# Performance work log

Hardware: AMD Instinct MI355X
Metric: run time of the kernel (lower is better)

## Reference

```python
import jax, jax.numpy as jnp
import numpy as np
import math

FIRE_THRESH = 0.85
SQRT_2_OVER_PI = math.sqrt(2.0 / math.pi)

def _gelu(x):
    # tanh-approx GELU, exactly as in the torch module
    return 0.5 * x * (1.0 + jnp.tanh(SQRT_2_OVER_PI * (x + 0.044715 * x * x * x)))

def setup_inputs() -> dict:
    key = jax.random.key(0)
    ks = jax.random.split(key, 8)
    B, T, D, N = 8, 4096, 1024, 512
    x = jax.random.normal(ks[0], (B, T, D), dtype=jnp.float32)
    log_beta = jnp.asarray(math.log(10.0), dtype=jnp.float32)
    log_k_inject = jnp.asarray(math.log(0.1), dtype=jnp.float32)
    # buffer keys are stored L2-normalized in the original module
    raw_keys = jax.random.normal(ks[1], (N, D), dtype=jnp.float32)
    buf_keys = raw_keys / jnp.maximum(jnp.linalg.norm(raw_keys, axis=-1, keepdims=True), 1e-12)
    buf_vals = jax.random.normal(ks[2], (N, D), dtype=jnp.float32)
    global_sum = jax.random.normal(ks[3], (D,), dtype=jnp.float32)
    mask = jnp.ones((N,), dtype=bool)
    hit_count = jax.random.randint(ks[4], (N,), 0, 100, dtype=jnp.int64 if jax.config.jax_enable_x64 else jnp.int32)
    n_global = 300
    return {"x": x, "log_beta": log_beta, "log_k_inject": log_k_inject,
            "buf_keys": buf_keys, "buf_vals": buf_vals, "global_sum": global_sum,
            "mask": mask, "hit_count": hit_count, "n_global": n_global}

def reference(x, log_beta, log_k_inject, buf_keys, buf_vals, global_sum, mask, hit_count, n_global):
    B, T, D = x.shape
    y = _gelu(x)  # [B,T,D]
    # m_curr = mean over all tokens, detached in the original
    m_curr = jax.lax.stop_gradient(jnp.mean(y.reshape(-1, D), axis=0))  # [D]
    beta = jnp.clip(jnp.exp(log_beta), 1.0, 50.0)
    k_inject = jnp.clip(jnp.exp(log_k_inject), 0.001, 2.0)
    # retrieval (no_grad block in torch)
    q = m_curr / jnp.maximum(jnp.linalg.norm(m_curr), 1e-12)  # [D]
    sims = buf_keys @ q                                        # [N]
    logits = jnp.where(mask, beta * sims, -1e9)
    attn = jax.nn.softmax(logits, axis=0)
    retrieved = attn @ buf_vals                                # [D]
    nearest_idx = jnp.argmax(logits)
    sims_plain = jnp.where(mask, sims, -1.0)
    hit = hit_count[nearest_idx] + (sims_plain[nearest_idx] > FIRE_THRESH).astype(hit_count.dtype)
    t = k_inject * jnp.log(hit.astype(x.dtype) + 1.0)
    global_mean = global_sum / max(int(n_global), 1)
    delta = jax.lax.stop_gradient(retrieved - global_mean)     # [D]
    return y + t * delta.reshape(1, 1, D)
```

## Files before the change

kernel.cpp:

```cpp
#include <hip/hip_runtime.h>
#include <math.h>

#define ROWS 32768
#define D    1024
#define DF4  256
#define NKEYS 512
#define CSB  512
#define CSR  64
#define R1B  16
#define RETB 8

__device__ __forceinline__ float gelu1(float x) {
    float z = 0.7978845608028654f * fmaf(0.044715f * x, x * x, x);
    float e = __expf(2.0f * z);
    return x - x / (e + 1.0f);
}

__global__ __launch_bounds__(256) void k_colsum(const float4* __restrict__ x4,
                                                float4* __restrict__ partial4) {
    int t = threadIdx.x, b = blockIdx.x;
    const float4* p = x4 + (size_t)b * CSR * DF4 + t;
    float4 acc = make_float4(0.f, 0.f, 0.f, 0.f);
#pragma unroll 8
    for (int r = 0; r < CSR; ++r) {
        float4 v = p[(size_t)r * DF4];
        acc.x += gelu1(v.x); acc.y += gelu1(v.y);
        acc.z += gelu1(v.z); acc.w += gelu1(v.w);
    }
    partial4[(size_t)b * DF4 + t] = acc;
}

__global__ __launch_bounds__(1024) void k_red1(const float* __restrict__ partial,
                                               float* __restrict__ partial2) {
    int d = threadIdx.x, b = blockIdx.x;
    float s = 0.f;
#pragma unroll
    for (int p = 0; p < 32; ++p) s += partial[(size_t)(b * 32 + p) * D + d];
    partial2[b * D + d] = s;
}

__global__ __launch_bounds__(1024) void k_q(const float* __restrict__ partial2,
                                            float* __restrict__ q) {
    __shared__ float red[1024];
    int d = threadIdx.x;
    float s = 0.f;
#pragma unroll
    for (int p = 0; p < R1B; ++p) s += partial2[p * D + d];
    float m = s * (1.0f / 32768.0f);
    red[d] = m * m;
    __syncthreads();
    for (int st = 512; st > 0; st >>= 1) {
        if (d < st) red[d] += red[d + st];
        __syncthreads();
    }
    float inv = 1.0f / fmaxf(sqrtf(red[0]), 1e-12f);
    q[d] = m * inv;
}

__global__ __launch_bounds__(256) void k_sims(const float4* __restrict__ keys4,
                                              const float4* __restrict__ q4,
                                              float* __restrict__ sims) {
    int n = blockIdx.x, t = threadIdx.x;
    float4 k = keys4[(size_t)n * DF4 + t];
    float4 qq = q4[t];
    float v = k.x * qq.x + k.y * qq.y + k.z * qq.z + k.w * qq.w;
#pragma unroll
    for (int off = 32; off > 0; off >>= 1) v += __shfl_down(v, off, 64);
    __shared__ float wsum[4];
    int wave = t >> 6, lane = t & 63;
    if (lane == 0) wsum[wave] = v;
    __syncthreads();
    if (t == 0) sims[n] = wsum[0] + wsum[1] + wsum[2] + wsum[3];
}

__global__ __launch_bounds__(256) void k_ret(const float* __restrict__ sims,
                                             const float4* __restrict__ vals4,
                                             const float* __restrict__ log_beta,
                                             const float* __restrict__ log_kinj,
                                             const int* __restrict__ hit_count,
                                             float* __restrict__ tval,
                                             float4* __restrict__ rp4) {
    int t = threadIdx.x, b = blockIdx.x;
    float beta = fminf(fmaxf(__expf(log_beta[0]), 1.0f), 50.0f);
    float s0 = sims[t], s1 = sims[t + 256];
    float l0 = beta * s0, l1 = beta * s1;

    __shared__ float red[256];
    red[t] = fmaxf(l0, l1);
    __syncthreads();
    for (int st = 128; st > 0; st >>= 1) {
        if (t < st) red[t] = fmaxf(red[t], red[t + st]);
        __syncthreads();
    }
    float lmax = red[0];
    __syncthreads();
    float e0 = __expf(l0 - lmax), e1 = __expf(l1 - lmax);
    red[t] = e0 + e1;
    __syncthreads();
    for (int st = 128; st > 0; st >>= 1) {
        if (t < st) red[t] += red[t + st];
        __syncthreads();
    }
    float inv_sum = 1.0f / red[0];
    __shared__ float w[NKEYS];
    w[t] = e0 * inv_sum;
    w[t + 256] = e1 * inv_sum;
    __syncthreads();

    if (b == 0) {
        __shared__ float amv[256];
        __shared__ int   ami[256];
        float v; int i;
        if (l1 > l0) { v = l1; i = t + 256; } else { v = l0; i = t; }
        amv[t] = v; ami[t] = i;
        __syncthreads();
        for (int st = 128; st > 0; st >>= 1) {
            if (t < st) {
                float ov = amv[t + st]; int oi = ami[t + st];
                if (ov > amv[t] || (ov == amv[t] && oi < ami[t])) { amv[t] = ov; ami[t] = oi; }
            }
            __syncthreads();
        }
        if (t == 0) {
            int nearest = ami[0];
            float sp = sims[nearest];
            int hit = hit_count[nearest] + (sp > 0.85f ? 1 : 0);
            float kinj = fminf(fmaxf(__expf(log_kinj[0]), 0.001f), 2.0f);
            tval[0] = kinj * logf((float)hit + 1.0f);
        }
    }

    float4 acc = make_float4(0.f, 0.f, 0.f, 0.f);
#pragma unroll 8
    for (int j = 0; j < 64; ++j) {
        int n = b * 64 + j;
        float a = w[n];
        float4 v = vals4[(size_t)n * DF4 + t];
        acc.x = fmaf(a, v.x, acc.x); acc.y = fmaf(a, v.y, acc.y);
        acc.z = fmaf(a, v.z, acc.z); acc.w = fmaf(a, v.w, acc.w);
    }
    rp4[(size_t)b * DF4 + t] = acc;
}

__global__ __launch_bounds__(256) void k_out(const float4* __restrict__ x4,
                                             const float4* __restrict__ rp4,
                                             const float4* __restrict__ gsum4,
                                             const int* __restrict__ ngl,
                                             const float* __restrict__ tval,
                                             float4* __restrict__ out4) {
    const int NF4 = ROWS * DF4;
    int i0 = blockIdx.x * 256 + threadIdx.x;
    int stride = gridDim.x * 256;
    int c = i0 & (DF4 - 1);

    float rx = 0.f, ry = 0.f, rz = 0.f, rw = 0.f;
#pragma unroll
    for (int bb = 0; bb < RETB; ++bb) {
        float4 v = rp4[bb * DF4 + c];
        rx += v.x; ry += v.y; rz += v.z; rw += v.w;
    }
    int ng = ngl[0];
    float invn = 1.0f / (float)(ng > 1 ? ng : 1);
    float tv = tval[0];
    float4 g = gsum4[c];
    float ax = tv * (rx - g.x * invn);
    float ay = tv * (ry - g.y * invn);
    float az = tv * (rz - g.z * invn);
    float aw = tv * (rw - g.w * invn);

    for (int i = i0; i < NF4; i += stride) {
        float4 v = x4[i];
        float4 o;
        o.x = gelu1(v.x) + ax;
        o.y = gelu1(v.y) + ay;
        o.z = gelu1(v.z) + az;
        o.w = gelu1(v.w) + aw;
        out4[i] = o;
    }
}

extern "C" void kernel_launch(void* const* d_in, const int* in_sizes, int n_in,
                              void* d_out, int out_size, void* d_ws, size_t ws_size,
                              hipStream_t stream) {
    const float* x          = (const float*)d_in[0];
    const float* log_beta   = (const float*)d_in[1];
    const float* log_kinj   = (const float*)d_in[2];
    const float* buf_keys   = (const float*)d_in[3];
    const float* buf_vals   = (const float*)d_in[4];
    const float* global_sum = (const float*)d_in[5];
    const int*   hit_count  = (const int*)d_in[7];
    const int*   n_global   = (const int*)d_in[8];
    float* out = (float*)d_out;

    float* ws = (float*)d_ws;
    float* partial  = ws;
    float* partial2 = partial + (size_t)CSB * D;
    float* q        = partial2 + R1B * D;
    float* sims     = q + D;
    float* tval     = sims + NKEYS;
    float* rp       = tval + 4;

    k_colsum<<<CSB, 256, 0, stream>>>((const float4*)x, (float4*)partial);
    k_red1 <<<R1B, 1024, 0, stream>>>(partial, partial2);
    k_q    <<<1, 1024, 0, stream>>>(partial2, q);
    k_sims <<<NKEYS, 256, 0, stream>>>((const float4*)buf_keys, (const float4*)q, sims);
    k_ret  <<<RETB, 256, 0, stream>>>(sims, (const float4*)buf_vals,
                                      log_beta, log_kinj, hit_count, tval, (float4*)rp);
    k_out  <<<2048, 256, 0, stream>>>((const float4*)x, (const float4*)rp,
                                      (const float4*)global_sum, n_global, tval,
                                      (float4*)out);
}
```

Before: 90.77 us.

## Cache GELU output as fp16 in first pass and fuse q normalization into sims

The first pass now writes GELU(x) as fp16 to workspace while computing column sums, and the output kernel reads these half values instead of re-reading fp32 x and recomputing GELU. This trades reading 128MB of x for writing and then reading 64MB of fp16, and drops the second GELU evaluation. It also merges the q normalization kernel into the similarity kernel, which removes one launch but recomputes the norm in every block. The fp16 storage of y adds rounding error to the output, and the new path runs only when the workspace is large enough.

```diff
diff --git a/kernel.cpp b/kernel.cpp
--- a/kernel.cpp
+++ b/kernel.cpp
@@ -1,4 +1,5 @@
 #include <hip/hip_runtime.h>
+#include <hip/hip_fp16.h>
 #include <math.h>
 
 #define ROWS 32768
@@ -14,6 +15,32 @@
     float z = 0.7978845608028654f * fmaf(0.044715f * x, x * x, x);
     float e = __expf(2.0f * z);
     return x - x / (e + 1.0f);
+}
+
+__device__ __forceinline__ short4 pack4(float a, float b, float c, float d) {
+    short4 r;
+    r.x = (short)__half_as_ushort(__float2half_rn(a));
+    r.y = (short)__half_as_ushort(__float2half_rn(b));
+    r.z = (short)__half_as_ushort(__float2half_rn(c));
+    r.w = (short)__half_as_ushort(__float2half_rn(d));
+    return r;
+}
+
+__global__ __launch_bounds__(256) void k_colsum_y(const float4* __restrict__ x4,
+                                                  float4* __restrict__ partial4,
+                                                  short4* __restrict__ y4) {
+    int t = threadIdx.x, b = blockIdx.x;
+    const float4* p = x4 + (size_t)b * CSR * DF4 + t;
+    short4* yp = y4 + (size_t)b * CSR * DF4 + t;
+    float4 acc = make_float4(0.f, 0.f, 0.f, 0.f);
+#pragma unroll 4
+    for (int r = 0; r < CSR; ++r) {
+        float4 v = p[(size_t)r * DF4];
+        float g0 = gelu1(v.x), g1 = gelu1(v.y), g2 = gelu1(v.z), g3 = gelu1(v.w);
+        acc.x += g0; acc.y += g1; acc.z += g2; acc.w += g3;
+        yp[(size_t)r * DF4] = pack4(g0, g1, g2, g3);
+    }
+    partial4[(size_t)b * DF4 + t] = acc;
 }
 
 __global__ __launch_bounds__(256) void k_colsum(const float4* __restrict__ x4,
@@ -39,38 +66,35 @@
     partial2[b * D + d] = s;
 }
 
-__global__ __launch_bounds__(1024) void k_q(const float* __restrict__ partial2,
-                                            float* __restrict__ q) {
-    __shared__ float red[1024];
-    int d = threadIdx.x;
-    float s = 0.f;
-#pragma unroll
-    for (int p = 0; p < R1B; ++p) s += partial2[p * D + d];
-    float m = s * (1.0f / 32768.0f);
-    red[d] = m * m;
-    __syncthreads();
-    for (int st = 512; st > 0; st >>= 1) {
-        if (d < st) red[d] += red[d + st];
-        __syncthreads();
-    }
-    float inv = 1.0f / fmaxf(sqrtf(red[0]), 1e-12f);
-    q[d] = m * inv;
-}
-
-__global__ __launch_bounds__(256) void k_sims(const float4* __restrict__ keys4,
-                                              const float4* __restrict__ q4,
+__global__ __launch_bounds__(256) void k_simq(const float4* __restrict__ partial2_4,
+                                              const float4* __restrict__ keys4,
                                               float* __restrict__ sims) {
     int n = blockIdx.x, t = threadIdx.x;
+    int wave = t >> 6, lane = t & 63;
+    float4 m4 = make_float4(0.f, 0.f, 0.f, 0.f);
+#pragma unroll
+    for (int p = 0; p < R1B; ++p) {
+        float4 v = partial2_4[p * DF4 + t];
+        m4.x += v.x; m4.y += v.y; m4.z += v.z; m4.w += v.w;
+    }
+    const float sc = 1.0f / 32768.0f;
+    m4.x *= sc; m4.y *= sc; m4.z *= sc; m4.w *= sc;
     float4 k = keys4[(size_t)n * DF4 + t];
-    float4 qq = q4[t];
-    float v = k.x * qq.x + k.y * qq.y + k.z * qq.z + k.w * qq.w;
-#pragma unroll
-    for (int off = 32; off > 0; off >>= 1) v += __shfl_down(v, off, 64);
-    __shared__ float wsum[4];
-    int wave = t >> 6, lane = t & 63;
-    if (lane == 0) wsum[wave] = v;
-    __syncthreads();
-    if (t == 0) sims[n] = wsum[0] + wsum[1] + wsum[2] + wsum[3];
+    float n2 = m4.x*m4.x + m4.y*m4.y + m4.z*m4.z + m4.w*m4.w;
+    float kd = k.x*m4.x + k.y*m4.y + k.z*m4.z + k.w*m4.w;
+#pragma unroll
+    for (int off = 32; off > 0; off >>= 1) {
+        n2 += __shfl_down(n2, off, 64);
+        kd += __shfl_down(kd, off, 64);
+    }
+    __shared__ float wn[4], wk[4];
+    if (lane == 0) { wn[wave] = n2; wk[wave] = kd; }
+    __syncthreads();
+    if (t == 0) {
+        float tn = wn[0] + wn[1] + wn[2] + wn[3];
+        float tk = wk[0] + wk[1] + wk[2] + wk[3];
+        sims[n] = tk / fmaxf(sqrtf(tn), 1e-12f);
+    }
 }
 
 __global__ __launch_bounds__(256) void k_ret(const float* __restrict__ sims,
@@ -133,26 +157,73 @@
     float4 acc = make_float4(0.f, 0.f, 0.f, 0.f);
 #pragma unroll 8
     for (int j = 0; j < 64; ++j) {
-        int n = b * 64 + j;
-        float a = w[n];
-        float4 v = vals4[(size_t)n * DF4 + t];
+        int nn = b * 64 + j;
+        float a = w[nn];
+        float4 v = vals4[(size_t)nn * DF4 + t];
         acc.x = fmaf(a, v.x, acc.x); acc.y = fmaf(a, v.y, acc.y);
         acc.z = fmaf(a, v.z, acc.z); acc.w = fmaf(a, v.w, acc.w);
     }
     rp4[(size_t)b * DF4 + t] = acc;
 }
 
-__global__ __launch_bounds__(256) void k_out(const float4* __restrict__ x4,
-                                             const float4* __restrict__ rp4,
-                                             const float4* __restrict__ gsum4,
-                                             const int* __restrict__ ngl,
-                                             const float* __restrict__ tval,
-                                             float4* __restrict__ out4) {
+__global__ __launch_bounds__(256) void k_out_y(const int4* __restrict__ y8,
+                                               const float4* __restrict__ rp4,
+                                               const float4* __restrict__ gsum4,
+                                               const int* __restrict__ ngl,
+                                               const float* __restrict__ tval,
+                                               float4* __restrict__ out4) {
+    const int NG = ROWS * 128;
+    int g0 = blockIdx.x * 256 + threadIdx.x;
+    int stride = gridDim.x * 256;
+    int c0 = (2 * g0) & (DF4 - 1);
+    int c1 = c0 + 1;
+
+    float4 r0 = make_float4(0.f,0.f,0.f,0.f), r1 = make_float4(0.f,0.f,0.f,0.f);
+#pragma unroll
+    for (int bb = 0; bb < RETB; ++bb) {
+        float4 a = rp4[bb * DF4 + c0];
+        float4 c = rp4[bb * DF4 + c1];
+        r0.x += a.x; r0.y += a.y; r0.z += a.z; r0.w += a.w;
+        r1.x += c.x; r1.y += c.y; r1.z += c.z; r1.w += c.w;
+    }
+    int ng = ngl[0];
+    float invn = 1.0f / (float)(ng > 1 ? ng : 1);
+    float tv = tval[0];
+    float4 gA = gsum4[c0], gB = gsum4[c1];
+    float4 A, B;
+    A.x = tv * (r0.x - gA.x * invn); A.y = tv * (r0.y - gA.y * invn);
+    A.z = tv * (r0.z - gA.z * invn); A.w = tv * (r0.w - gA.w * invn);
+    B.x = tv * (r1.x - gB.x * invn); B.y = tv * (r1.y - gB.y * invn);
+    B.z = tv * (r1.z - gB.z * invn); B.w = tv * (r1.w - gB.w * invn);
+
+    for (int g = g0; g < NG; g += stride) {
+        int4 yv = y8[g];
+        __half2 h01 = *reinterpret_cast<const __half2*>(&yv.x);
+        __half2 h23 = *reinterpret_cast<const __half2*>(&yv.y);
+        __half2 h45 = *reinterpret_cast<const __half2*>(&yv.z);
+        __half2 h67 = *reinterpret_cast<const __half2*>(&yv.w);
+        float2 f01 = __half22float2(h01);
+        float2 f23 = __half22float2(h23);
+        float2 f45 = __half22float2(h45);
+        float2 f67 = __half22float2(h67);
+        float4 o1, o2;
+        o1.x = f01.x + A.x; o1.y = f01.y + A.y; o1.z = f23.x + A.z; o1.w = f23.y + A.w;
+        o2.x = f45.x + B.x; o2.y = f45.y + B.y; o2.z = f67.x + B.z; o2.w = f67.y + B.w;
+        out4[2 * g]     = o1;
+        out4[2 * g + 1] = o2;
+    }
+}
+
+__global__ __launch_bounds__(256) void k_out_x(const float4* __restrict__ x4,
+                                               const float4* __restrict__ rp4,
+                                               const float4* __restrict__ gsum4,
+                                               const int* __restrict__ ngl,
+                                               const float* __restrict__ tval,
+                                               float4* __restrict__ out4) {
     const int NF4 = ROWS * DF4;
     int i0 = blockIdx.x * 256 + threadIdx.x;
     int stride = gridDim.x * 256;
     int c = i0 & (DF4 - 1);
-
     float rx = 0.f, ry = 0.f, rz = 0.f, rw = 0.f;
 #pragma unroll
     for (int bb = 0; bb < RETB; ++bb) {
@@ -167,7 +238,6 @@
     float ay = tv * (ry - g.y * invn);
     float az = tv * (rz - g.z * invn);
     float aw = tv * (rw - g.w * invn);
-
     for (int i = i0; i < NF4; i += stride) {
         float4 v = x4[i];
         float4 o;
@@ -192,21 +262,34 @@
     const int*   n_global   = (const int*)d_in[8];
     float* out = (float*)d_out;
 
-    float* ws = (float*)d_ws;
-    float* partial  = ws;
-    float* partial2 = partial + (size_t)CSB * D;
-    float* q        = partial2 + R1B * D;
-    float* sims     = q + D;
-    float* tval     = sims + NKEYS;
-    float* rp       = tval + 4;
-
-    k_colsum<<<CSB, 256, 0, stream>>>((const float4*)x, (float4*)partial);
+    const size_t Y_BYTES = (size_t)ROWS * D * 2;
+    bool use_y = ws_size >= Y_BYTES + (8u << 20);
+
+    char* wsb = (char*)d_ws;
+    short4* y      = (short4*)wsb;
+    float* partial = (float*)(wsb + (use_y ? Y_BYTES : 0));
+    float* partial2= partial + (size_t)CSB * D;
+    float* sims    = partial2 + R1B * D;
+    float* tval    = sims + NKEYS;
+    float* rp      = tval + 4;
+
+    if (use_y) {
+        k_colsum_y<<<CSB, 256, 0, stream>>>((const float4*)x, (float4*)partial, y);
+    } else {
+        k_colsum  <<<CSB, 256, 0, stream>>>((const float4*)x, (float4*)partial);
+    }
     k_red1 <<<R1B, 1024, 0, stream>>>(partial, partial2);
-    k_q    <<<1, 1024, 0, stream>>>(partial2, q);
-    k_sims <<<NKEYS, 256, 0, stream>>>((const float4*)buf_keys, (const float4*)q, sims);
+    k_simq <<<NKEYS, 256, 0, stream>>>((const float4*)partial2, (const float4*)buf_keys,
+                                       sims);
     k_ret  <<<RETB, 256, 0, stream>>>(sims, (const float4*)buf_vals,
                                       log_beta, log_kinj, hit_count, tval, (float4*)rp);
-    k_out  <<<2048, 256, 0, stream>>>((const float4*)x, (const float4*)rp,
-                                      (const float4*)global_sum, n_global, tval,
-                                      (float4*)out);
-}
+    if (use_y) {
+        k_out_y<<<2048, 256, 0, stream>>>((const int4*)y, (const float4*)rp,
+                                          (const float4*)global_sum, n_global, tval,
+                                          (float4*)out);
+    } else {
+        k_out_x<<<2048, 256, 0, stream>>>((const float4*)x, (const float4*)rp,
+                                          (const float4*)global_sum, n_global, tval,
+                                          (float4*)out);
+    }
+}
```

Result: slower. 119.1 us (+31.2%).
